# Optimization experiments

Hardware: AMD Instinct MI355X
Metric: run time of the kernel (lower is better)

Reference implementation:

```python
import jax, jax.numpy as jnp
import numpy as np

TABLE_SIZE = 2 ** 18  # log2_hashmap_size = 18
N_LEVELS = 8
PRIME_Y = np.uint32(2654435761)
PRIME_Z = np.uint32(805459861)
# 8 cube-corner offsets in {0,1}^3
CORNERS = jnp.asarray([[(c >> d) & 1 for d in range(3)] for c in range(8)], dtype=jnp.int32)  # [8,3]


def setup_inputs() -> dict:
    key = jax.random.key(0)
    ks = jax.random.split(key, 6)
    N = 2_097_152
    x = jax.random.uniform(ks[0], (N, 3), dtype=jnp.float32)          # points in [0,1]^3
    mesh_min = jnp.zeros((3,), jnp.float32)
    mesh_max = jnp.ones((3,), jnp.float32)
    # tcnn initializes grid features uniform in [-1e-4, 1e-4]
    tables = jax.random.uniform(ks[1], (N_LEVELS, TABLE_SIZE, 2), jnp.float32, -1e-4, 1e-4)
    w_in = jax.random.normal(ks[2], (16, 64), jnp.float32) * (1.0 / np.sqrt(16))
    w_hidden = jax.random.normal(ks[3], (3, 64, 64), jnp.float32) * (1.0 / np.sqrt(64))
    w_out = jax.random.normal(ks[4], (64, 1), jnp.float32) * (1.0 / np.sqrt(64))
    return {"x": x, "mesh_min": mesh_min, "mesh_max": mesh_max,
            "tables": tables, "w_in": w_in, "w_hidden": w_hidden, "w_out": w_out}


def _hashgrid_encode(u, tables):
    """u: [N,3] in [0,1]. tables: [L, T, F]. Returns [N, L*F]."""
    feats = []
    for l in range(N_LEVELS):
        res = 2 * (2 ** l)  # base_resolution=2, per_level_scale=2
        pos = u * res                                   # [N,3]
        c0 = jnp.floor(pos).astype(jnp.int32)
        w = pos - c0                                    # trilinear fractions, [N,3]
        corners = jnp.clip(c0[:, None, :] + CORNERS[None], 0, res)  # [N,8,3]
        if (res + 1) ** 3 <= TABLE_SIZE:
            # dense grid: no hashing needed at coarse levels
            idx = (corners[..., 0]
                   + corners[..., 1] * (res + 1)
                   + corners[..., 2] * (res + 1) ** 2)
        else:
            uc = corners.astype(jnp.uint32)
            h = uc[..., 0] ^ (uc[..., 1] * PRIME_Y) ^ (uc[..., 2] * PRIME_Z)
            idx = (h % jnp.uint32(TABLE_SIZE)).astype(jnp.int32)
        # trilinear weights per corner: prod over dims of w or (1-w)
        wt = jnp.prod(jnp.where(CORNERS[None] == 1, w[:, None, :], 1.0 - w[:, None, :]), axis=-1)  # [N,8]
        feats.append(jnp.einsum('nc,ncf->nf', wt, tables[l][idx]))  # [N,F]
    return jnp.concatenate(feats, axis=-1)  # [N, L*F] = [N,16]


def reference(x, mesh_min, mesh_max, tables, w_in, w_hidden, w_out):
    u = (x - mesh_min) / (mesh_max - mesh_min)          # normalize to [0,1]^3
    enc = _hashgrid_encode(u, tables)                   # [N,16]
    h = jax.nn.relu(enc @ w_in)                         # [N,64]
    for i in range(w_hidden.shape[0]):                  # 3 more hidden layers (4 total)
        h = jax.nn.relu(h @ w_hidden[i])
    out = (h @ w_out).squeeze(-1)                       # [N], no output activation
    return out
```

## Files before the change

kernel.cpp:

```cpp
#include <hip/hip_runtime.h>
#include <stdint.h>

typedef _Float16 half2v __attribute__((ext_vector_type(2)));
typedef _Float16 half4 __attribute__((ext_vector_type(4)));
typedef _Float16 half8 __attribute__((ext_vector_type(8)));
typedef float floatx4 __attribute__((ext_vector_type(4)));
typedef float float4u __attribute__((ext_vector_type(4), aligned(8)));

#define TPB 256
#define ENC_ROW 20

__device__ __forceinline__ half2v pkrtz(float a, float b) {
    return __builtin_bit_cast(half2v, __builtin_amdgcn_cvt_pkrtz(a, b));
}

__device__ __forceinline__ half4 relu_pack(floatx4 c) {
    half2v lo = pkrtz(fmaxf(c[0], 0.f), fmaxf(c[1], 0.f));
    half2v hi = pkrtz(fmaxf(c[2], 0.f), fmaxf(c[3], 0.f));
    half4 r;
    r[0] = lo[0]; r[1] = lo[1]; r[2] = hi[0]; r[3] = hi[1];
    return r;
}

__global__ void prep_all(const float* __restrict__ tables,
                         uint32_t* __restrict__ tf,
                         const float* __restrict__ w_in,
                         const float* __restrict__ w_hidden,
                         _Float16* __restrict__ ws) {
    int b = blockIdx.x;
    if (b < 8192) {
        int i = b * 256 + threadIdx.x;
        float2 v = ((const float2*)tables)[i];
        half2v h;
        h[0] = (_Float16)(v.x * 8192.f);
        h[1] = (_Float16)(v.y * 8192.f);
        tf[i] = __builtin_bit_cast(uint32_t, h);
    } else {
        int i = (b - 8192) * 256 + threadIdx.x;
        if (i < 1024) {
            int j = i & 3, lane = (i >> 2) & 63, mt = i >> 8;
            int k = ((lane >> 4) & 3) * 4 + j;
            int n = mt * 16 + (lane & 15);
            ws[i] = (_Float16)w_in[k * 64 + n];
        } else if (i < 13312) {
            int t = i - 1024;
            int j = t & 3, lane = (t >> 2) & 63;
            int mt = (t >> 8) & 3, kt = (t >> 10) & 3, layer = t >> 12;
            int k = kt * 16 + ((lane >> 4) & 3) * 4 + j;
            int n = mt * 16 + (lane & 15);
            ws[i] = (_Float16)w_hidden[layer * 4096 + k * 64 + n];
        }
    }
}

__global__ void prep_weights(const float* __restrict__ w_in,
                             const float* __restrict__ w_hidden,
                             _Float16* __restrict__ ws) {
    int i = blockIdx.x * 256 + threadIdx.x;
    if (i < 1024) {
        int j = i & 3, lane = (i >> 2) & 63, mt = i >> 8;
        int k = ((lane >> 4) & 3) * 4 + j;
        int n = mt * 16 + (lane & 15);
        ws[i] = (_Float16)w_in[k * 64 + n];
    } else if (i < 13312) {
        int t = i - 1024;
        int j = t & 3, lane = (t >> 2) & 63;
        int mt = (t >> 8) & 3, kt = (t >> 10) & 3, layer = t >> 12;
        int k = kt * 16 + ((lane >> 4) & 3) * 4 + j;
        int n = mt * 16 + (lane & 15);
        ws[i] = (_Float16)w_hidden[layer * 4096 + k * 64 + n];
    }
}

__global__ __launch_bounds__(TPB, 4) void fused_kernel(
    const float* __restrict__ x,
    const float* __restrict__ mesh_min,
    const float* __restrict__ mesh_max,
    const float* __restrict__ tables,
    const uint32_t* __restrict__ tabs,
    const _Float16* __restrict__ ws,
    const float* __restrict__ w_out,
    float* __restrict__ out,
    int N) {
    __shared__ __align__(16) char smem[26700];
    float2* ltab = (float2*)smem;
    uint32_t* l3tab = (uint32_t*)(smem + 7048);
    _Float16 (*encbuf)[64][ENC_ROW] = (_Float16 (*)[64][ENC_ROW])smem;

    const int wave = threadIdx.x >> 6;
    const int lane = threadIdx.x & 63;
    const int l15 = lane & 15;
    const int quad = lane >> 4;
    const int wavebase = blockIdx.x * TPB + wave * 64;
    const int p = wavebase + lane;

    {
        const float2* t0 = (const float2*)tables;
        for (int i = threadIdx.x; i < 27; i += TPB) ltab[i] = t0[i];
        const float2* t1 = (const float2*)(tables + 1 * 524288);
        for (int i = threadIdx.x; i < 125; i += TPB) ltab[27 + i] = t1[i];
        const float2* t2 = (const float2*)(tables + 2 * 524288);
        for (int i = threadIdx.x; i < 729; i += TPB) ltab[152 + i] = t2[i];
        const uint32_t* t3 = tabs + 3 * 262144;
        for (int i = threadIdx.x; i < 4913; i += TPB) l3tab[i] = t3[i];
    }

    float mn0 = mesh_min[0], mn1 = mesh_min[1], mn2 = mesh_min[2];
    float mx0 = mesh_max[0], mx1 = mesh_max[1], mx2 = mesh_max[2];
    float ux = (x[3 * p + 0] - mn0) / (mx0 - mn0);
    float uy = (x[3 * p + 1] - mn1) / (mx1 - mn1);
    float uz = (x[3 * p + 2] - mn2) / (mx2 - mn2);

    float ef[16];
    float wl[3][3];
    uint32_t g[24];
    uint32_t g4[8];
    float w4x, w4y, w4z;

#pragma unroll
    for (int l = 0; l < 3; ++l) {
        const int res = 64 << l;
        const uint32_t* tab = tabs + (size_t)(l + 5) * 262144;
        float px = ux * (float)res, py = uy * (float)res, pz = uz * (float)res;
        int cx = (int)floorf(px), cy = (int)floorf(py), cz = (int)floorf(pz);
        wl[l][0] = px - (float)cx;
        wl[l][1] = py - (float)cy;
        wl[l][2] = pz - (float)cz;
        uint32_t hy0 = (uint32_t)cy * 2654435761u, hy1 = (uint32_t)(cy + 1) * 2654435761u;
        uint32_t hz0 = (uint32_t)cz * 805459861u,  hz1 = (uint32_t)(cz + 1) * 805459861u;
#pragma unroll
        for (int c = 0; c < 4; ++c) {
            uint32_t hyz = ((c & 1) ? hy1 : hy0) ^ ((c & 2) ? hz1 : hz0);
            uint32_t i0 = ((uint32_t)cx ^ hyz) & 262143u;
            uint32_t i1 = ((uint32_t)(cx + 1) ^ hyz) & 262143u;
            g[l * 8 + 2 * c + 0] = tab[i0];
            g[l * 8 + 2 * c + 1] = tab[i1];
        }
    }

    {
        const int s = 33;
        const uint32_t* tab = tabs + (size_t)4 * 262144;
        float px = ux * 32.f, py = uy * 32.f, pz = uz * 32.f;
        int cx = (int)floorf(px), cy = (int)floorf(py), cz = (int)floorf(pz);
        w4x = px - (float)cx; w4y = py - (float)cy; w4z = pz - (float)cz;
#pragma unroll
        for (int c = 0; c < 4; ++c) {
            int Y = cy + ((c & 1) ? 1 : 0);
            int Z = cz + ((c & 2) ? 1 : 0);
            int i0 = cx + Y * s + Z * s * s;
            g4[2 * c + 0] = tab[i0];
            g4[2 * c + 1] = tab[i0 + 1];
        }
    }

    __syncthreads();

#pragma unroll
    for (int l = 0; l < 3; ++l) {
        const int res = 2 << l;
        const int s = res + 1;
        const int base = (l == 0) ? 0 : (l == 1) ? 27 : 152;
        float px = ux * (float)res, py = uy * (float)res, pz = uz * (float)res;
        int cx = (int)floorf(px), cy = (int)floorf(py), cz = (int)floorf(pz);
        float wx = px - (float)cx, wy = py - (float)cy, wz = pz - (float)cz;
        float f0 = 0.f, f1 = 0.f;
#pragma unroll
        for (int c = 0; c < 4; ++c) {
            int i0 = base + cx + (cy + ((c & 1) ? 1 : 0)) * s + (cz + ((c & 2) ? 1 : 0)) * s * s;
            float wyz = ((c & 1) ? wy : 1.f - wy) * ((c & 2) ? wz : 1.f - wz);
            float2 e0 = ltab[i0];
            float2 e1 = ltab[i0 + 1];
            f0 += wyz * (e0.x + wx * (e1.x - e0.x));
            f1 += wyz * (e0.y + wx * (e1.y - e0.y));
        }
        ef[2 * l + 0] = f0 * 8192.f;
        ef[2 * l + 1] = f1 * 8192.f;
    }

    {
        const int s = 17;
        float px = ux * 16.f, py = uy * 16.f, pz = uz * 16.f;
        int cx = (int)floorf(px), cy = (int)floorf(py), cz = (int)floorf(pz);
        float wx = px - (float)cx, wy = py - (float)cy, wz = pz - (float)cz;
        float f0 = 0.f, f1 = 0.f;
#pragma unroll
        for (int c = 0; c < 4; ++c) {
            int i0 = cx + (cy + ((c & 1) ? 1 : 0)) * s + (cz + ((c & 2) ? 1 : 0)) * s * s;
            float wyz = ((c & 1) ? wy : 1.f - wy) * ((c & 2) ? wz : 1.f - wz);
            half2v e0 = __builtin_bit_cast(half2v, l3tab[i0]);
            half2v e1 = __builtin_bit_cast(half2v, l3tab[i0 + 1]);
            f0 += wyz * ((float)e0[0] + wx * ((float)e1[0] - (float)e0[0]));
            f1 += wyz * ((float)e0[1] + wx * ((float)e1[1] - (float)e0[1]));
        }
        ef[6] = f0;
        ef[7] = f1;
    }

    {
        float f0 = 0.f, f1 = 0.f;
#pragma unroll
        for (int c = 0; c < 4; ++c) {
            float wyz = ((c & 1) ? w4y : 1.f - w4y) * ((c & 2) ? w4z : 1.f - w4z);
            half2v e0 = __builtin_bit_cast(half2v, g4[2 * c + 0]);
            half2v e1 = __builtin_bit_cast(half2v, g4[2 * c + 1]);
            f0 += wyz * ((float)e0[0] + w4x * ((float)e1[0] - (float)e0[0]));
            f1 += wyz * ((float)e0[1] + w4x * ((float)e1[1] - (float)e0[1]));
        }
        ef[8] = f0;
        ef[9] = f1;
    }

#pragma unroll
    for (int l = 0; l < 3; ++l) {
        float wx = wl[l][0], wy = wl[l][1], wz = wl[l][2];
        float f0 = 0.f, f1 = 0.f;
#pragma unroll
        for (int c = 0; c < 4; ++c) {
            float wyz = ((c & 1) ? wy : 1.f - wy) * ((c & 2) ? wz : 1.f - wz);
            half2v e0 = __builtin_bit_cast(half2v, g[l * 8 + 2 * c + 0]);
            half2v e1 = __builtin_bit_cast(half2v, g[l * 8 + 2 * c + 1]);
            f0 += wyz * ((float)e0[0] + wx * ((float)e1[0] - (float)e0[0]));
            f1 += wyz * ((float)e0[1] + wx * ((float)e1[1] - (float)e0[1]));
        }
        ef[10 + 2 * l + 0] = f0;
        ef[10 + 2 * l + 1] = f1;
    }

    __syncthreads();

#pragma unroll
    for (int v = 0; v < 4; ++v) {
        half2v lo = pkrtz(ef[4 * v + 0], ef[4 * v + 1]);
        half2v hi = pkrtz(ef[4 * v + 2], ef[4 * v + 3]);
        half4 t;
        t[0] = lo[0]; t[1] = lo[1]; t[2] = hi[0]; t[3] = hi[1];
        *(half4*)&encbuf[wave][lane][v * 4] = t;
    }

    floatx4 C[4][4];
    {
        half4 b[4];
#pragma unroll
        for (int nt = 0; nt < 4; ++nt)
            b[nt] = *(const half4*)&encbuf[wave][nt * 16 + l15][quad * 4];
#pragma unroll
        for (int mt = 0; mt < 4; ++mt) {
            half4 a = *(const half4*)(ws + mt * 256 + lane * 4);
#pragma unroll
            for (int nt = 0; nt < 4; ++nt) {
                floatx4 zero = {0.f, 0.f, 0.f, 0.f};
                C[mt][nt] = __builtin_amdgcn_mfma_f32_16x16x16f16(a, b[nt], zero, 0, 0, 0);
            }
        }
    }

#pragma unroll
    for (int layer = 0; layer < 3; ++layer) {
        half4 b[4][4];
#pragma unroll
        for (int kt = 0; kt < 4; ++kt)
#pragma unroll
            for (int nt = 0; nt < 4; ++nt)
                b[kt][nt] = relu_pack(C[kt][nt]);
#pragma unroll
        for (int mt = 0; mt < 4; ++mt) {
            half4 a[4];
#pragma unroll
            for (int kt = 0; kt < 4; ++kt)
                a[kt] = *(const half4*)(ws + 1024 + ((layer * 4 + kt) * 4 + mt) * 256 + lane * 4);
#pragma unroll
            for (int nt = 0; nt < 4; ++nt) {
                floatx4 acc = {0.f, 0.f, 0.f, 0.f};
#pragma unroll
                for (int kt = 0; kt < 4; ++kt)
                    acc = __builtin_amdgcn_mfma_f32_16x16x16f16(a[kt], b[kt][nt], acc, 0, 0, 0);
                C[mt][nt] = acc;
            }
        }
    }

    {
        float s[4] = {0.f, 0.f, 0.f, 0.f};
#pragma unroll
        for (int mt = 0; mt < 4; ++mt) {
            float4 wo = *(const float4*)(w_out + mt * 16 + quad * 4);
#pragma unroll
            for (int nt = 0; nt < 4; ++nt) {
                s[nt] = fmaf(fmaxf(C[mt][nt][0], 0.f), wo.x, s[nt]);
                s[nt] = fmaf(fmaxf(C[mt][nt][1], 0.f), wo.y, s[nt]);
                s[nt] = fmaf(fmaxf(C[mt][nt][2], 0.f), wo.z, s[nt]);
                s[nt] = fmaf(fmaxf(C[mt][nt][3], 0.f), wo.w, s[nt]);
            }
        }
#pragma unroll
        for (int nt = 0; nt < 4; ++nt) {
            s[nt] += __shfl_xor(s[nt], 16, 64);
            s[nt] += __shfl_xor(s[nt], 32, 64);
        }
        float r = (quad & 1) ? ((quad & 2) ? s[3] : s[1])
                             : ((quad & 2) ? s[2] : s[0]);
        out[wavebase + quad * 16 + l15] = r * (1.f / 8192.f);
    }
}

__global__ __launch_bounds__(TPB, 4) void hashgrid_mlp_kernel(
    const float* __restrict__ x,
    const float* __restrict__ mesh_min,
    const float* __restrict__ mesh_max,
    const float* __restrict__ tables,
    const _Float16* __restrict__ ws,
    const float* __restrict__ w_out,
    float* __restrict__ out,
    int N) {
    __shared__ float2 ltab[881];
    __shared__ _Float16 encbuf[4][64][ENC_ROW];

    const int wave = threadIdx.x >> 6;
    const int lane = threadIdx.x & 63;
    const int l15 = lane & 15;
    const int quad = lane >> 4;
    const int wavebase = blockIdx.x * TPB + wave * 64;
    const int p = wavebase + lane;

    {
        const float2* t0 = (const float2*)tables;
        for (int i = threadIdx.x; i < 27; i += TPB) ltab[i] = t0[i];
        const float2* t1 = (const float2*)(tables + 1 * 524288);
        for (int i = threadIdx.x; i < 125; i += TPB) ltab[27 + i] = t1[i];
        const float2* t2 = (const float2*)(tables + 2 * 524288);
        for (int i = threadIdx.x; i < 729; i += TPB) ltab[152 + i] = t2[i];
    }

    float mn0 = mesh_min[0], mn1 = mesh_min[1], mn2 = mesh_min[2];
    float mx0 = mesh_max[0], mx1 = mesh_max[1], mx2 = mesh_max[2];
    float ux = (x[3 * p + 0] - mn0) / (mx0 - mn0);
    float uy = (x[3 * p + 1] - mn1) / (mx1 - mn1);
    float uz = (x[3 * p + 2] - mn2) / (mx2 - mn2);

    float ef[16];
    float wl[3][3];
    float2 g[24];

#pragma unroll
    for (int l = 0; l < 3; ++l) {
        const int res = 64 << l;
        const float* tab = tables + (size_t)(l + 5) * 524288;
        float px = ux * (float)res, py = uy * (float)res, pz = uz * (float)res;
        int cx = (int)floorf(px), cy = (int)floorf(py), cz = (int)floorf(pz);
        wl[l][0] = px - (float)cx;
        wl[l][1] = py - (float)cy;
        wl[l][2] = pz - (float)cz;
        uint32_t hy0 = (uint32_t)cy * 2654435761u, hy1 = (uint32_t)(cy + 1) * 2654435761u;
        uint32_t hz0 = (uint32_t)cz * 805459861u,  hz1 = (uint32_t)(cz + 1) * 805459861u;
#pragma unroll
        for (int c = 0; c < 4; ++c) {
            uint32_t hyz = ((c & 1) ? hy1 : hy0) ^ ((c & 2) ? hz1 : hz0);
            uint32_t i0 = ((uint32_t)cx ^ hyz) & 262143u;
            uint32_t i1 = ((uint32_t)(cx + 1) ^ hyz) & 262143u;
            g[l * 8 + 2 * c + 0] = *(const float2*)(tab + 2 * (size_t)i0);
            g[l * 8 + 2 * c + 1] = *(const float2*)(tab + 2 * (size_t)i1);
        }
    }

#pragma unroll
    for (int l = 3; l < 5; ++l) {
        const int res = 2 << l;
        const int s = res + 1;
        const float* tab = tables + (size_t)l * 524288;
        float px = ux * (float)res, py = uy * (float)res, pz = uz * (float)res;
        int cx = (int)floorf(px), cy = (int)floorf(py), cz = (int)floorf(pz);
        float wx = px - (float)cx, wy = py - (float)cy, wz = pz - (float)cz;
        float f0 = 0.f, f1 = 0.f;
#pragma unroll
        for (int c = 0; c < 4; ++c) {
            int Y = cy + ((c & 1) ? 1 : 0);
            int Z = cz + ((c & 2) ? 1 : 0);
            float wyz = ((c & 1) ? wy : 1.f - wy) * ((c & 2) ? wz : 1.f - wz);
            int i0 = cx + Y * s + Z * s * s;
            float4u v = *(const float4u*)(tab + 2 * (size_t)i0);
            f0 += wyz * (v.x + wx * (v.z - v.x));
            f1 += wyz * (v.y + wx * (v.w - v.y));
        }
        ef[2 * l + 0] = f0;
        ef[2 * l + 1] = f1;
    }

    __syncthreads();

#pragma unroll
    for (int l = 0; l < 3; ++l) {
        const int res = 2 << l;
        const int s = res + 1;
        const int base = (l == 0) ? 0 : (l == 1) ? 27 : 152;
        float px = ux * (float)res, py = uy * (float)res, pz = uz * (float)res;
        int cx = (int)floorf(px), cy = (int)floorf(py), cz = (int)floorf(pz);
        float wx = px - (float)cx, wy = py - (float)cy, wz = pz - (float)cz;
        float f0 = 0.f, f1 = 0.f;
#pragma unroll
        for (int c = 0; c < 4; ++c) {
            int i0 = base + cx + (cy + ((c & 1) ? 1 : 0)) * s + (cz + ((c & 2) ? 1 : 0)) * s * s;
            float wyz = ((c & 1) ? wy : 1.f - wy) * ((c & 2) ? wz : 1.f - wz);
            float2 e0 = ltab[i0];
            float2 e1 = ltab[i0 + 1];
            f0 += wyz * (e0.x + wx * (e1.x - e0.x));
            f1 += wyz * (e0.y + wx * (e1.y - e0.y));
        }
        ef[2 * l + 0] = f0;
        ef[2 * l + 1] = f1;
    }

#pragma unroll
    for (int l = 0; l < 3; ++l) {
        float wx = wl[l][0], wy = wl[l][1], wz = wl[l][2];
        float f0 = 0.f, f1 = 0.f;
#pragma unroll
        for (int c = 0; c < 4; ++c) {
            float wyz = ((c & 1) ? wy : 1.f - wy) * ((c & 2) ? wz : 1.f - wz);
            float2 e0 = g[l * 8 + 2 * c + 0];
            float2 e1 = g[l * 8 + 2 * c + 1];
            f0 += wyz * (e0.x + wx * (e1.x - e0.x));
            f1 += wyz * (e0.y + wx * (e1.y - e0.y));
        }
        ef[10 + 2 * l + 0] = f0;
        ef[10 + 2 * l + 1] = f1;
    }

#pragma unroll
    for (int v = 0; v < 4; ++v) {
        half2v lo = pkrtz(ef[4 * v + 0] * 8192.f, ef[4 * v + 1] * 8192.f);
        half2v hi = pkrtz(ef[4 * v + 2] * 8192.f, ef[4 * v + 3] * 8192.f);
        half4 t;
        t[0] = lo[0]; t[1] = lo[1]; t[2] = hi[0]; t[3] = hi[1];
        *(half4*)&encbuf[wave][lane][v * 4] = t;
    }

    floatx4 C[4][4];
    {
        half4 b[4];
#pragma unroll
        for (int nt = 0; nt < 4; ++nt)
            b[nt] = *(const half4*)&encbuf[wave][nt * 16 + l15][quad * 4];
#pragma unroll
        for (int mt = 0; mt < 4; ++mt) {
            half4 a = *(const half4*)(ws + mt * 256 + lane * 4);
#pragma unroll
            for (int nt = 0; nt < 4; ++nt) {
                floatx4 zero = {0.f, 0.f, 0.f, 0.f};
                C[mt][nt] = __builtin_amdgcn_mfma_f32_16x16x16f16(a, b[nt], zero, 0, 0, 0);
            }
        }
    }

#pragma unroll
    for (int layer = 0; layer < 3; ++layer) {
        half4 b[4][4];
#pragma unroll
        for (int kt = 0; kt < 4; ++kt)
#pragma unroll
            for (int nt = 0; nt < 4; ++nt)
                b[kt][nt] = relu_pack(C[kt][nt]);
#pragma unroll
        for (int mt = 0; mt < 4; ++mt) {
            half4 a[4];
#pragma unroll
            for (int kt = 0; kt < 4; ++kt)
                a[kt] = *(const half4*)(ws + 1024 + ((layer * 4 + kt) * 4 + mt) * 256 + lane * 4);
#pragma unroll
            for (int nt = 0; nt < 4; ++nt) {
                floatx4 acc = {0.f, 0.f, 0.f, 0.f};
#pragma unroll
                for (int kt = 0; kt < 4; ++kt)
                    acc = __builtin_amdgcn_mfma_f32_16x16x16f16(a[kt], b[kt][nt], acc, 0, 0, 0);
                C[mt][nt] = acc;
            }
        }
    }

    {
        float s[4] = {0.f, 0.f, 0.f, 0.f};
#pragma unroll
        for (int mt = 0; mt < 4; ++mt) {
            float4 wo = *(const float4*)(w_out + mt * 16 + quad * 4);
#pragma unroll
            for (int nt = 0; nt < 4; ++nt) {
                s[nt] = fmaf(fmaxf(C[mt][nt][0], 0.f), wo.x, s[nt]);
                s[nt] = fmaf(fmaxf(C[mt][nt][1], 0.f), wo.y, s[nt]);
                s[nt] = fmaf(fmaxf(C[mt][nt][2], 0.f), wo.z, s[nt]);
                s[nt] = fmaf(fmaxf(C[mt][nt][3], 0.f), wo.w, s[nt]);
            }
        }
#pragma unroll
        for (int nt = 0; nt < 4; ++nt) {
            s[nt] += __shfl_xor(s[nt], 16, 64);
            s[nt] += __shfl_xor(s[nt], 32, 64);
        }
        float r = (quad & 1) ? ((quad & 2) ? s[3] : s[1])
                             : ((quad & 2) ? s[2] : s[0]);
        out[wavebase + quad * 16 + l15] = r * (1.f / 8192.f);
    }
}

extern "C" void kernel_launch(void* const* d_in, const int* in_sizes, int n_in,
                              void* d_out, int out_size, void* d_ws,
                              size_t ws_size, hipStream_t stream) {
    const float* x        = (const float*)d_in[0];
    const float* mesh_min = (const float*)d_in[1];
    const float* mesh_max = (const float*)d_in[2];
    const float* tables   = (const float*)d_in[3];
    const float* w_in     = (const float*)d_in[4];
    const float* w_hidden = (const float*)d_in[5];
    const float* w_out    = (const float*)d_in[6];
    float* out = (float*)d_out;
    _Float16* ws = (_Float16*)d_ws;

    int N = out_size;

    size_t need = 32768 + (size_t)8 * 262144 * 4;
    if (ws_size >= need) {
        uint32_t* tf = (uint32_t*)((char*)d_ws + 32768);
        hipLaunchKernelGGL(prep_all, dim3(8244), dim3(256), 0, stream,
                           tables, tf, w_in, w_hidden, ws);
        hipLaunchKernelGGL(fused_kernel, dim3(N / TPB), dim3(TPB), 0, stream,
                           x, mesh_min, mesh_max, tables, tf, ws, w_out, out, N);
    } else {
        hipLaunchKernelGGL(prep_weights, dim3(52), dim3(256), 0, stream,
                           w_in, w_hidden, ws);
        hipLaunchKernelGGL(hashgrid_mlp_kernel, dim3(N / TPB), dim3(TPB), 0, stream,
                           x, mesh_min, mesh_max, tables, ws, w_out, out, N);
    }
}
```

Measured before the change: 269.9 us.

## Cut register pressure: pack encodings early, recompute fractions, split MLP into halves

Trilinear features are packed to fp16 pairs right after computation, so only 8 live registers hold them instead of 16 floats. Fractional weights for the hashed levels are recomputed after the gathers instead of being kept live across them. The MLP now processes the 64 points of a wave in two halves of 32, which halves the accumulator tile held in registers. The goal is to lower VGPR usage, allow more waves in flight, and hide gather latency, at the cost of reloading the weights once per half and a little extra ALU work.

After: 268.1 us. Within noise of the previous version (-0.7%).

```diff
diff --git a/kernel.cpp b/kernel.cpp
--- a/kernel.cpp
+++ b/kernel.cpp
@@ -3,13 +3,15 @@
 
 typedef _Float16 half2v __attribute__((ext_vector_type(2)));
 typedef _Float16 half4 __attribute__((ext_vector_type(4)));
-typedef _Float16 half8 __attribute__((ext_vector_type(8)));
 typedef float floatx4 __attribute__((ext_vector_type(4)));
 typedef float float4u __attribute__((ext_vector_type(4), aligned(8)));
 
 #define TPB 256
 #define ENC_ROW 20
 
+__device__ __forceinline__ uint32_t pkrtz_u32(float a, float b) {
+    return __builtin_bit_cast(uint32_t, __builtin_amdgcn_cvt_pkrtz(a, b));
+}
 __device__ __forceinline__ half2v pkrtz(float a, float b) {
     return __builtin_bit_cast(half2v, __builtin_amdgcn_cvt_pkrtz(a, b));
 }
@@ -31,10 +33,7 @@
     if (b < 8192) {
         int i = b * 256 + threadIdx.x;
         float2 v = ((const float2*)tables)[i];
-        half2v h;
-        h[0] = (_Float16)(v.x * 8192.f);
-        h[1] = (_Float16)(v.y * 8192.f);
-        tf[i] = __builtin_bit_cast(uint32_t, h);
+        tf[i] = pkrtz_u32(v.x * 8192.f, v.y * 8192.f);
     } else {
         int i = (b - 8192) * 256 + threadIdx.x;
         if (i < 1024) {
@@ -111,21 +110,17 @@
     float uy = (x[3 * p + 1] - mn1) / (mx1 - mn1);
     float uz = (x[3 * p + 2] - mn2) / (mx2 - mn2);
 
-    float ef[16];
-    float wl[3][3];
+    uint32_t e[8];
     uint32_t g[24];
     uint32_t g4[8];
-    float w4x, w4y, w4z;
 
 #pragma unroll
     for (int l = 0; l < 3; ++l) {
         const int res = 64 << l;
         const uint32_t* tab = tabs + (size_t)(l + 5) * 262144;
-        float px = ux * (float)res, py = uy * (float)res, pz = uz * (float)res;
-        int cx = (int)floorf(px), cy = (int)floorf(py), cz = (int)floorf(pz);
-        wl[l][0] = px - (float)cx;
-        wl[l][1] = py - (float)cy;
-        wl[l][2] = pz - (float)cz;
+        int cx = (int)floorf(ux * (float)res);
+        int cy = (int)floorf(uy * (float)res);
+        int cz = (int)floorf(uz * (float)res);
         uint32_t hy0 = (uint32_t)cy * 2654435761u, hy1 = (uint32_t)(cy + 1) * 2654435761u;
         uint32_t hz0 = (uint32_t)cz * 805459861u,  hz1 = (uint32_t)(cz + 1) * 805459861u;
 #pragma unroll
@@ -141,9 +136,9 @@
     {
         const int s = 33;
         const uint32_t* tab = tabs + (size_t)4 * 262144;
-        float px = ux * 32.f, py = uy * 32.f, pz = uz * 32.f;
-        int cx = (int)floorf(px), cy = (int)floorf(py), cz = (int)floorf(pz);
-        w4x = px - (float)cx; w4y = py - (float)cy; w4z = pz - (float)cz;
+        int cx = (int)floorf(ux * 32.f);
+        int cy = (int)floorf(uy * 32.f);
+        int cz = (int)floorf(uz * 32.f);
 #pragma unroll
         for (int c = 0; c < 4; ++c) {
             int Y = cy + ((c & 1) ? 1 : 0);
@@ -174,8 +169,7 @@
             f0 += wyz * (e0.x + wx * (e1.x - e0.x));
             f1 += wyz * (e0.y + wx * (e1.y - e0.y));
         }
-        ef[2 * l + 0] = f0 * 8192.f;
-        ef[2 * l + 1] = f1 * 8192.f;
+        e[l] = pkrtz_u32(f0 * 8192.f, f1 * 8192.f);
     }
 
     {
@@ -193,27 +187,31 @@
             f0 += wyz * ((float)e0[0] + wx * ((float)e1[0] - (float)e0[0]));
             f1 += wyz * ((float)e0[1] + wx * ((float)e1[1] - (float)e0[1]));
         }
-        ef[6] = f0;
-        ef[7] = f1;
-    }
-
-    {
-        float f0 = 0.f, f1 = 0.f;
-#pragma unroll
-        for (int c = 0; c < 4; ++c) {
-            float wyz = ((c & 1) ? w4y : 1.f - w4y) * ((c & 2) ? w4z : 1.f - w4z);
+        e[3] = pkrtz_u32(f0, f1);
+    }
+
+    {
+        float wx = ux * 32.f; wx -= floorf(wx);
+        float wy = uy * 32.f; wy -= floorf(wy);
+        float wz = uz * 32.f; wz -= floorf(wz);
+        float f0 = 0.f, f1 = 0.f;
+#pragma unroll
+        for (int c = 0; c < 4; ++c) {
+            float wyz = ((c & 1) ? wy : 1.f - wy) * ((c & 2) ? wz : 1.f - wz);
             half2v e0 = __builtin_bit_cast(half2v, g4[2 * c + 0]);
             half2v e1 = __builtin_bit_cast(half2v, g4[2 * c + 1]);
-            f0 += wyz * ((float)e0[0] + w4x * ((float)e1[0] - (float)e0[0]));
-            f1 += wyz * ((float)e0[1] + w4x * ((float)e1[1] - (float)e0[1]));
-        }
-        ef[8] = f0;
-        ef[9] = f1;
+            f0 += wyz * ((float)e0[0] + wx * ((float)e1[0] - (float)e0[0]));
+            f1 += wyz * ((float)e0[1] + wx * ((float)e1[1] - (float)e0[1]));
+        }
+        e[4] = pkrtz_u32(f0, f1);
     }
 
 #pragma unroll
     for (int l = 0; l < 3; ++l) {
-        float wx = wl[l][0], wy = wl[l][1], wz = wl[l][2];
+        const float res = (float)(64 << l);
+        float wx = ux * res; wx -= floorf(wx);
+        float wy = uy * res; wy -= floorf(wy);
+        float wz = uz * res; wz -= floorf(wz);
         float f0 = 0.f, f1 = 0.f;
 #pragma unroll
         for (int c = 0; c < 4; ++c) {
@@ -223,83 +221,87 @@
             f0 += wyz * ((float)e0[0] + wx * ((float)e1[0] - (float)e0[0]));
             f1 += wyz * ((float)e0[1] + wx * ((float)e1[1] - (float)e0[1]));
         }
-        ef[10 + 2 * l + 0] = f0;
-        ef[10 + 2 * l + 1] = f1;
+        e[5 + l] = pkrtz_u32(f0, f1);
     }
 
     __syncthreads();
 
-#pragma unroll
-    for (int v = 0; v < 4; ++v) {
-        half2v lo = pkrtz(ef[4 * v + 0], ef[4 * v + 1]);
-        half2v hi = pkrtz(ef[4 * v + 2], ef[4 * v + 3]);
-        half4 t;
-        t[0] = lo[0]; t[1] = lo[1]; t[2] = hi[0]; t[3] = hi[1];
-        *(half4*)&encbuf[wave][lane][v * 4] = t;
-    }
-
-    floatx4 C[4][4];
-    {
-        half4 b[4];
-#pragma unroll
-        for (int nt = 0; nt < 4; ++nt)
-            b[nt] = *(const half4*)&encbuf[wave][nt * 16 + l15][quad * 4];
-#pragma unroll
-        for (int mt = 0; mt < 4; ++mt) {
-            half4 a = *(const half4*)(ws + mt * 256 + lane * 4);
-#pragma unroll
-            for (int nt = 0; nt < 4; ++nt) {
+    {
+        _Float16* row = &encbuf[wave][lane][0];
+        uint2* r2 = (uint2*)row;
+        uint2 t;
+        t.x = e[0]; t.y = e[1]; r2[0] = t;
+        t.x = e[2]; t.y = e[3]; r2[1] = t;
+        t.x = e[4]; t.y = e[5]; r2[2] = t;
+        t.x = e[6]; t.y = e[7]; r2[3] = t;
+    }
+
+    float sacc[4];
+#pragma unroll
+    for (int h = 0; h < 2; ++h) {
+        floatx4 C[4][2];
+        {
+            half4 b0 = *(const half4*)&encbuf[wave][(2 * h + 0) * 16 + l15][quad * 4];
+            half4 b1 = *(const half4*)&encbuf[wave][(2 * h + 1) * 16 + l15][quad * 4];
+#pragma unroll
+            for (int mt = 0; mt < 4; ++mt) {
+                half4 a = *(const half4*)(ws + mt * 256 + lane * 4);
                 floatx4 zero = {0.f, 0.f, 0.f, 0.f};
-                C[mt][nt] = __builtin_amdgcn_mfma_f32_16x16x16f16(a, b[nt], zero, 0, 0, 0);
-            }
-        }
-    }
-
-#pragma unroll
-    for (int layer = 0; layer < 3; ++layer) {
-        half4 b[4][4];
-#pragma unroll
-        for (int kt = 0; kt < 4; ++kt)
-#pragma unroll
-            for (int nt = 0; nt < 4; ++nt)
-                b[kt][nt] = relu_pack(C[kt][nt]);
-#pragma unroll
-        for (int mt = 0; mt < 4; ++mt) {
-            half4 a[4];
-#pragma unroll
-            for (int kt = 0; kt < 4; ++kt)
-                a[kt] = *(const half4*)(ws + 1024 + ((layer * 4 + kt) * 4 + mt) * 256 + lane * 4);
-#pragma unroll
-            for (int nt = 0; nt < 4; ++nt) {
-                floatx4 acc = {0.f, 0.f, 0.f, 0.f};
+                C[mt][0] = __builtin_amdgcn_mfma_f32_16x16x16f16(a, b0, zero, 0, 0, 0);
+                C[mt][1] = __builtin_amdgcn_mfma_f32_16x16x16f16(a, b1, zero, 0, 0, 0);
+            }
+        }
+#pragma unroll
+        for (int layer = 0; layer < 3; ++layer) {
+            half4 b[4][2];
+#pragma unroll
+            for (int kt = 0; kt < 4; ++kt) {
+                b[kt][0] = relu_pack(C[kt][0]);
+                b[kt][1] = relu_pack(C[kt][1]);
+            }
+#pragma unroll
+            for (int mt = 0; mt < 4; ++mt) {
+                half4 a[4];
 #pragma unroll
                 for (int kt = 0; kt < 4; ++kt)
-                    acc = __builtin_amdgcn_mfma_f32_16x16x16f16(a[kt], b[kt][nt], acc, 0, 0, 0);
-                C[mt][nt] = acc;
-            }
-        }
-    }
-
-    {
-        float s[4] = {0.f, 0.f, 0.f, 0.f};
-#pragma unroll
-        for (int mt = 0; mt < 4; ++mt) {
-            float4 wo = *(const float4*)(w_out + mt * 16 + quad * 4);
-#pragma unroll
-            for (int nt = 0; nt < 4; ++nt) {
-                s[nt] = fmaf(fmaxf(C[mt][nt][0], 0.f), wo.x, s[nt]);
-                s[nt] = fmaf(fmaxf(C[mt][nt][1], 0.f), wo.y, s[nt]);
-                s[nt] = fmaf(fmaxf(C[mt][nt][2], 0.f), wo.z, s[nt]);
-                s[nt] = fmaf(fmaxf(C[mt][nt][3], 0.f), wo.w, s[nt]);
-            }
-        }
+                    a[kt] = *(const half4*)(ws + 1024 + ((layer * 4 + kt) * 4 + mt) * 256 + lane * 4);
+#pragma unroll
+                for (int j = 0; j < 2; ++j) {
+                    floatx4 acc = {0.f, 0.f, 0.f, 0.f};
+#pragma unroll
+                    for (int kt = 0; kt < 4; ++kt)
+                        acc = __builtin_amdgcn_mfma_f32_16x16x16f16(a[kt], b[kt][j], acc, 0, 0, 0);
+                    C[mt][j] = acc;
+                }
+            }
+        }
+        {
+            float s0 = 0.f, s1 = 0.f;
+#pragma unroll
+            for (int mt = 0; mt < 4; ++mt) {
+                float4 wo = *(const float4*)(w_out + mt * 16 + quad * 4);
+                s0 = fmaf(fmaxf(C[mt][0][0], 0.f), wo.x, s0);
+                s0 = fmaf(fmaxf(C[mt][0][1], 0.f), wo.y, s0);
+                s0 = fmaf(fmaxf(C[mt][0][2], 0.f), wo.z, s0);
+                s0 = fmaf(fmaxf(C[mt][0][3], 0.f), wo.w, s0);
+                s1 = fmaf(fmaxf(C[mt][1][0], 0.f), wo.x, s1);
+                s1 = fmaf(fmaxf(C[mt][1][1], 0.f), wo.y, s1);
+                s1 = fmaf(fmaxf(C[mt][1][2], 0.f), wo.z, s1);
+                s1 = fmaf(fmaxf(C[mt][1][3], 0.f), wo.w, s1);
+            }
+            sacc[2 * h + 0] = s0;
+            sacc[2 * h + 1] = s1;
+        }
+    }
+
+    {
 #pragma unroll
         for (int nt = 0; nt < 4; ++nt) {
-            s[nt] += __shfl_xor(s[nt], 16, 64);
-            s[nt] += __shfl_xor(s[nt], 32, 64);
-        }
-        float r = (quad & 1) ? ((quad & 2) ? s[3] : s[1])
-                             : ((quad & 2) ? s[2] : s[0]);
+            sacc[nt] += __shfl_xor(sacc[nt], 16, 64);
+            sacc[nt] += __shfl_xor(sacc[nt], 32, 64);
+        }
+        float r = (quad & 1) ? ((quad & 2) ? sacc[3] : sacc[1])
+                             : ((quad & 2) ? sacc[2] : sacc[0]);
         out[wavebase + quad * 16 + l15] = r * (1.f / 8192.f);
     }
 }
```
